# Optimization experiments

Measured on AMD Instinct MI355X. Metric: run time of the kernel, lower is better.

## Reference

```python
import jax, jax.numpy as jnp
import numpy as np

B, T, P, H, D = 2, 2048, 1024, 16, 128
C = H * D  # 2048
ROPE_THETA = 10000.0


def setup_inputs() -> dict:
    key = jax.random.key(0)
    ks = jax.random.split(key, 5)
    x = jax.random.normal(ks[0], (B, T, C), jnp.float32)
    w_qkv = jax.random.normal(ks[1], (C, 3 * C), jnp.float32) * 0.02  # Linear(dim, 3*dim), applied as x @ w
    w_out = jax.random.normal(ks[2], (C, C), jnp.float32) * 0.02
    past_k = jax.random.normal(ks[3], (B, H, P, D), jnp.float32)
    past_v = jax.random.normal(ks[4], (B, H, P, D), jnp.float32)
    return {"x": x, "w_qkv": w_qkv, "w_out": w_out, "past_k": past_k, "past_v": past_v}


def _rope(q, k, offset):
    # rotate-half RoPE (GPT-NeoX style), positions offset..offset+T-1
    d = q.shape[-1]
    inv_freq = 1.0 / (ROPE_THETA ** (jnp.arange(0, d, 2, dtype=jnp.float32) / d))  # [d/2]
    pos = offset + jnp.arange(q.shape[2], dtype=jnp.float32)                        # [T]
    ang = pos[:, None] * inv_freq[None, :]                                          # [T, d/2]
    cos = jnp.concatenate([jnp.cos(ang), jnp.cos(ang)], -1)[None, None]             # [1,1,T,d]
    sin = jnp.concatenate([jnp.sin(ang), jnp.sin(ang)], -1)[None, None]

    def rot_half(t):
        t1, t2 = jnp.split(t, 2, axis=-1)
        return jnp.concatenate([-t2, t1], -1)

    return q * cos + rot_half(q) * sin, k * cos + rot_half(k) * sin


def reference(x, w_qkv, w_out, past_k, past_v):
    Bv, Tv, Cv = x.shape
    Hn = past_k.shape[1]
    Dd = Cv // Hn
    # fused QKV projection
    qkv = x @ w_qkv                       # [B,T,3C]
    q, k, v = jnp.split(qkv, 3, axis=-1)  # each [B,T,C]

    def split_heads(t):
        return t.reshape(Bv, Tv, Hn, Dd).transpose(0, 2, 1, 3)  # [B,H,T,D]

    q, k, v = split_heads(q), split_heads(k), split_heads(v)
    # RoPE with offset = past length
    q, k = _rope(q, k, past_k.shape[2])
    # KV-cache concat along time axis
    k = jnp.concatenate([past_k, k], axis=2)  # [B,H,P+T,D]
    v = jnp.concatenate([past_v, v], axis=2)
    # SDPA: past_kv present -> is_causal=False, no mask (full attention)
    scale = 1.0 / jnp.sqrt(jnp.float32(Dd))
    scores = jnp.einsum('bhqd,bhkd->bhqk', q, k) * scale
    attn = jax.nn.softmax(scores, axis=-1)
    out = jnp.einsum('bhqk,bhkd->bhqd', attn, v)
    out = out.transpose(0, 2, 1, 3).reshape(Bv, Tv, Cv)
    return out @ w_out
```

## Files before the change

kernel.cpp:

```cpp
#include <hip/hip_runtime.h>
#include <stdint.h>

#define B_ 2
#define T_ 2048
#define P_ 1024
#define H_ 16
#define D_ 128
#define C_ 2048
#define S_ 3072
#define M_ 4096
#define N3_ 6144

typedef unsigned short u16;
typedef unsigned int uint32;
typedef __attribute__((ext_vector_type(8))) short short8;
typedef __attribute__((ext_vector_type(8))) __bf16 bf16x8;
typedef __attribute__((ext_vector_type(4))) float f32x4;
typedef __attribute__((ext_vector_type(16))) float f32x16;
typedef __attribute__((ext_vector_type(4))) unsigned short u16x4;
typedef __attribute__((ext_vector_type(4))) unsigned int uint4v;

static __device__ __forceinline__ float bf2f(u16 h) {
    union { unsigned int u; float f; } x; x.u = ((unsigned int)h) << 16; return x.f;
}
static __device__ __forceinline__ u16 f2bf(float f) {
    return __builtin_bit_cast(u16, (__bf16)f);
}
static __device__ __forceinline__ uint32 pkbf(float x, float y) {
    return (uint32)f2bf(x) | ((uint32)f2bf(y) << 16);
}

static __device__ __forceinline__ f32x4 mfma_bf16(short8 a, short8 b, f32x4 c) {
    return __builtin_amdgcn_mfma_f32_16x16x32_bf16(
        __builtin_bit_cast(bf16x8, a), __builtin_bit_cast(bf16x8, b), c, 0, 0, 0);
}
static __device__ __forceinline__ f32x16 mfma32(short8 a, short8 b, f32x16 c) {
    return __builtin_amdgcn_mfma_f32_32x32x16_bf16(
        __builtin_bit_cast(bf16x8, a), __builtin_bit_cast(bf16x8, b), c, 0, 0, 0);
}

typedef __attribute__((address_space(3))) unsigned int lds_u32;
typedef const __attribute__((address_space(1))) unsigned int glb_u32;
static __device__ __forceinline__ void gload_lds16(const void* g, void* l) {
    __builtin_amdgcn_global_load_lds((glb_u32*)g, (lds_u32*)l, 16, 0, 0);
}

static __device__ __forceinline__ void storeC(float* p, float v) { *p = v; }
static __device__ __forceinline__ void storeC(u16* p, float v) { *p = f2bf(v); }


__global__ void castx_kernel(const float* __restrict__ x, u16* __restrict__ Xb) {
    int idx = blockIdx.x * 256 + threadIdx.x;
    const float4 v = ((const float4*)x)[idx];
    u16x4 o;
    o.x = f2bf(v.x); o.y = f2bf(v.y); o.z = f2bf(v.z); o.w = f2bf(v.w);
    ((u16x4*)Xb)[idx] = o;
}

__global__ void wT_kernel(const float* __restrict__ W, u16* __restrict__ Wt,
                          int Ndim, int Kdim) {
    __shared__ float tile[64][65];
    const int n0 = blockIdx.x * 64, k0 = blockIdx.y * 64;
    const int tid = threadIdx.x;
#pragma unroll
    for (int i = 0; i < 16; i++) {
        int idx = tid + i * 256;
        int r = idx >> 6, c = idx & 63;
        tile[r][c] = W[(size_t)(k0 + r) * Ndim + n0 + c];
    }
    __syncthreads();
#pragma unroll
    for (int i = 0; i < 16; i++) {
        int idx = tid + i * 256;
        int r = idx >> 6, c = idx & 63;
        Wt[(size_t)(n0 + r) * Kdim + k0 + c] = f2bf(tile[c][r]);
    }
}

__global__ void rope_table_kernel(float* __restrict__ cosT, float* __restrict__ sinT) {
    int idx = blockIdx.x * 256 + threadIdx.x;
    int t = idx >> 6, d = idx & 63;
    float inv = powf(10000.0f, -(float)d * (1.0f / 64.0f));
    float ang = (float)(P_ + t) * inv;
    cosT[idx] = cosf(ang);
    sinT[idx] = sinf(ang);
}

__global__ void rope_qk_kernel(u16* __restrict__ QKVb, u16* __restrict__ Kc,
                               const float* __restrict__ cosT,
                               const float* __restrict__ sinT) {
    int idx = blockIdx.x * 256 + threadIdx.x;
    int d = idx & 63;
    int h = (idx >> 6) & 15;
    int t = (idx >> 10) & 2047;
    int b = idx >> 21;
    size_t rowoff = (size_t)(b * T_ + t) * N3_;
    float c = cosT[(t << 6) + d], s = sinT[(t << 6) + d];
    {
        u16* p1 = QKVb + rowoff + h * 128 + d;
        float x1 = bf2f(p1[0]), x2 = bf2f(p1[64]);
        p1[0]  = f2bf(x1 * c - x2 * s);
        p1[64] = f2bf(x2 * c + x1 * s);
    }
    {
        const u16* p1 = QKVb + rowoff + C_ + h * 128 + d;
        float x1 = bf2f(p1[0]), x2 = bf2f(p1[64]);
        u16* o = Kc + ((size_t)(b * H_ + h) * S_ + P_ + t) * 128 + d;
        o[0]  = f2bf(x1 * c - x2 * s);
        o[64] = f2bf(x2 * c + x1 * s);
    }
}

__global__ void pastk_kernel(const float* __restrict__ past_k, u16* __restrict__ Kc) {
    int idx = blockIdx.x * 256 + threadIdx.x;
    int d = idx & 127;
    int p = (idx >> 7) & 1023;
    int bh = idx >> 17;
    Kc[((size_t)bh * S_ + p) * 128 + d] = f2bf(past_k[idx]);
}

__global__ void vnewT_kernel(const u16* __restrict__ QKVb, u16* __restrict__ Vt) {
    __shared__ u16 tile[64][65];
    const int t0 = blockIdx.x * 64, d0 = blockIdx.y * 64, bh = blockIdx.z;
    const int b = bh >> 4, h = bh & 15;
    const int tid = threadIdx.x;
#pragma unroll
    for (int i = 0; i < 16; i++) {
        int idx = tid + i * 256;
        int r = idx >> 6, c = idx & 63;
        tile[r][c] = QKVb[(size_t)(b * T_ + t0 + r) * N3_ + 2 * C_ + h * 128 + d0 + c];
    }
    __syncthreads();
#pragma unroll
    for (int i = 0; i < 16; i++) {
        int idx = tid + i * 256;
        int r = idx >> 6, c = idx & 63;
        Vt[((size_t)bh * 128 + d0 + r) * S_ + P_ + t0 + c] = tile[c][r];
    }
}

__global__ void vpastT_kernel(const float* __restrict__ past_v, u16* __restrict__ Vt) {
    __shared__ float tile[64][65];
    const int p0 = blockIdx.x * 64, d0 = blockIdx.y * 64, bh = blockIdx.z;
    const int tid = threadIdx.x;
#pragma unroll
    for (int i = 0; i < 16; i++) {
        int idx = tid + i * 256;
        int r = idx >> 6, c = idx & 63;
        tile[r][c] = past_v[((size_t)bh * P_ + p0 + r) * 128 + d0 + c];
    }
    __syncthreads();
#pragma unroll
    for (int i = 0; i < 16; i++) {
        int idx = tid + i * 256;
        int r = idx >> 6, c = idx & 63;
        Vt[((size_t)bh * 128 + d0 + r) * S_ + p0 + c] = f2bf(tile[c][r]);
    }
}

template <typename OutT>
__global__ void __launch_bounds__(512, 1)
gemm3(const u16* __restrict__ A, const u16* __restrict__ Bt,
      OutT* __restrict__ Co, int Mdim, int Ndim, int Kdim) {
    __shared__ u16 lA[3 * 256 * 64];
    __shared__ u16 lB[3 * 128 * 64];
    const int nbx = Ndim >> 7;
    const int nwg = (Mdim >> 8) * nbx;
    int bid = blockIdx.x;
    int wg = (bid & 7) * (nwg >> 3) + (bid >> 3);
    const int bm = wg / nbx, bn = wg % nbx;
    const int m0 = bm << 8, n0 = bn << 7;
    const int tid = threadIdx.x;
    const int wave = tid >> 6, lane = tid & 63;
    const int mw = wave >> 1, nw = wave & 1;
    const int l15 = lane & 15, l4 = lane >> 4;

    f32x4 acc[4][4];
#pragma unroll
    for (int i = 0; i < 4; i++)
#pragma unroll
        for (int j = 0; j < 4; j++) acc[i][j] = (f32x4){0.f, 0.f, 0.f, 0.f};

    const u16* aSrc[4];
    const u16* bSrc[2];
#pragma unroll
    for (int i = 0; i < 4; i++) {
        int cid = i * 512 + tid;
        int r = cid >> 3, pc = cid & 7;
        aSrc[i] = A + (size_t)(m0 + r) * Kdim + ((pc ^ (r & 7)) << 3);
    }
#pragma unroll
    for (int i = 0; i < 2; i++) {
        int cid = i * 512 + tid;
        int r = cid >> 3, pc = cid & 7;
        bSrc[i] = Bt + (size_t)(n0 + r) * Kdim + ((pc ^ (r & 7)) << 3);
    }

#define STAGE3(bi, kt) do {                                                     \
    u16* _pa = lA + (bi) * 16384 + wave * 512;                                  \
    u16* _pb = lB + (bi) * 8192 + wave * 512;                                   \
    _Pragma("unroll")                                                           \
    for (int i = 0; i < 4; i++)                                                 \
        gload_lds16(aSrc[i] + (size_t)(kt) * 64, _pa + i * 4096);               \
    _Pragma("unroll")                                                           \
    for (int i = 0; i < 2; i++)                                                 \
        gload_lds16(bSrc[i] + (size_t)(kt) * 64, _pb + i * 4096);               \
} while (0)

    STAGE3(0, 0);
    STAGE3(1, 1);

    const int NT = Kdim >> 6;
    int bc = 0;
    for (int t = 0; t < NT; ++t) {
        if (t + 1 < NT) asm volatile("s_waitcnt vmcnt(6)" ::: "memory");
        else            asm volatile("s_waitcnt vmcnt(0)" ::: "memory");
        __builtin_amdgcn_s_barrier();
        asm volatile("" ::: "memory");
        if (t + 2 < NT) {
            int b2 = bc + 2; if (b2 >= 3) b2 -= 3;
            STAGE3(b2, t + 2);
        }
        const u16* la = lA + bc * 16384;
        const u16* lb = lB + bc * 8192;
        short8 af[4][2], bf[4][2];
#pragma unroll
        for (int i = 0; i < 4; i++)
#pragma unroll
            for (int kk = 0; kk < 2; kk++) {
                int r = mw * 64 + i * 16 + l15;
                int cb = (kk * 64 + l4 * 16) ^ ((r & 7) << 4);
                af[i][kk] = *(const short8*)&la[r * 64 + (cb >> 1)];
            }
#pragma unroll
        for (int j = 0; j < 4; j++)
#pragma unroll
            for (int kk = 0; kk < 2; kk++) {
                int r = nw * 64 + j * 16 + l15;
                int cb = (kk * 64 + l4 * 16) ^ ((r & 7) << 4);
                bf[j][kk] = *(const short8*)&lb[r * 64 + (cb >> 1)];
            }
        __builtin_amdgcn_s_setprio(1);
#pragma unroll
        for (int kk = 0; kk < 2; kk++)
#pragma unroll
            for (int i = 0; i < 4; i++)
#pragma unroll
                for (int j = 0; j < 4; j++)
                    acc[i][j] = mfma_bf16(af[i][kk], bf[j][kk], acc[i][j]);
        __builtin_amdgcn_s_setprio(0);
        __builtin_amdgcn_sched_barrier(0);
        bc = bc + 1; if (bc >= 3) bc = 0;
    }
#undef STAGE3

#pragma unroll
    for (int i = 0; i < 4; i++)
#pragma unroll
        for (int j = 0; j < 4; j++) {
            int row = m0 + mw * 64 + i * 16 + (l4 << 2);
            int col = n0 + nw * 64 + j * 16 + l15;
#pragma unroll
            for (int q = 0; q < 4; q++)
                storeC(&Co[(size_t)(row + q) * Ndim + col], acc[i][j][q]);
        }
}

__global__ void __launch_bounds__(256, 2)
attn_kernel(const u16* __restrict__ QKVb, const u16* __restrict__ Kc,
            const u16* __restrict__ Vt, u16* __restrict__ O) {
    __shared__ u16 ldsK[2][64 * 128];
    __shared__ u16 ldsV[2][128 * 64];

    int bid = blockIdx.x;
    int wg = (bid & 7) * 64 + (bid >> 3);
    const int qc = wg & 15;
    const int bh = wg >> 4;
    const int b = bh >> 4, h = bh & 15;
    const int tid = threadIdx.x, wave = tid >> 6, lane = tid & 63;
    const int l31 = lane & 31, hi = lane >> 5;

    const int krow = tid >> 4;
    const int kcol = (((tid & 15) << 4) ^ ((krow & 7) << 4)) >> 1;
    const int vrow = tid >> 3;
    const int vcol = (((tid & 7) << 4) ^ ((vrow & 7) << 4)) >> 1;

    const u16* Kbh = Kc + (size_t)bh * S_ * 128;
    const u16* Vbh = Vt + (size_t)bh * 128 * S_;

    const int tq = qc * 128 + wave * 32 + l31;
    short8 qf[8];
    {
        const u16* qp = QKVb + (size_t)(b * T_ + tq) * N3_ + h * 128 + hi * 8;
#pragma unroll
        for (int ks = 0; ks < 8; ks++) qf[ks] = *(const short8*)(qp + ks * 16);
    }

    f32x16 acco[4];
#pragma unroll
    for (int d = 0; d < 4; d++) acco[d] = (f32x16)(0.0f);
    float mrow = -1e30f, lrow = 0.f;
    const float sl2 = 0.08838834764831845f * 1.4426950408889634f;

#define STAGE(bufi, tt) do {                                                    \
    const int _s0 = (tt) * 64;                                                  \
    _Pragma("unroll")                                                           \
    for (int i = 0; i < 4; i++)                                                 \
        gload_lds16(Kbh + (size_t)(_s0 + krow + i * 16) * 128 + kcol,           \
                    (char*)&ldsK[bufi][0] + i * 4096 + wave * 1024);            \
    _Pragma("unroll")                                                           \
    for (int i = 0; i < 4; i++)                                                 \
        gload_lds16(Vbh + (size_t)(vrow + i * 32) * S_ + _s0 + vcol,            \
                    (char*)&ldsV[bufi][0] + i * 4096 + wave * 1024);            \
} while (0)

    STAGE(0, 0);
    __syncthreads();

    const int swz = (l31 & 7) << 4;

    for (int t = 0; t < S_ / 64; ++t) {
        const int cur = t & 1;
        if (t < S_ / 64 - 1) STAGE(cur ^ 1, t + 1);

        const u16* Kl = ldsK[cur];
        const u16* Vl = ldsV[cur];

        f32x16 p0 = (f32x16)(0.0f), p1 = (f32x16)(0.0f);
        __builtin_amdgcn_s_setprio(1);
#pragma unroll
        for (int ks = 0; ks < 8; ks++) {
            const int cidx = (((ks * 32 + hi * 16) ^ swz) >> 1);
            short8 k0 = *(const short8*)&Kl[(l31 << 7) + cidx];
            short8 k1 = *(const short8*)&Kl[((32 + l31) << 7) + cidx];
            p0 = mfma32(k0, qf[ks], p0);
            p1 = mfma32(k1, qf[ks], p1);
        }
        __builtin_amdgcn_s_setprio(0);

        float pm = fmaxf(p0[0], p0[1]);
#pragma unroll
        for (int r = 2; r < 16; r++) pm = fmaxf(pm, p0[r]);
#pragma unroll
        for (int r = 0; r < 16; r++) pm = fmaxf(pm, p1[r]);
        pm = fmaxf(pm, __shfl_xor(pm, 32));
        float pmS = pm * sl2;
        if (!__all(pmS <= mrow + 8.0f)) {
            float mn = fmaxf(mrow, pmS);
            float fac = exp2f(mrow - mn);
            mrow = mn;
            lrow *= fac;
#pragma unroll
            for (int d = 0; d < 4; d++)
#pragma unroll
                for (int r = 0; r < 16; r++) acco[d][r] *= fac;
        }
        float sum = 0.f;
#pragma unroll
        for (int r = 0; r < 16; r++) { p0[r] = exp2f(fmaf(p0[r], sl2, -mrow)); sum += p0[r]; }
#pragma unroll
        for (int r = 0; r < 16; r++) { p1[r] = exp2f(fmaf(p1[r], sl2, -mrow)); sum += p1[r]; }
        sum += __shfl_xor(sum, 32);
        lrow += sum;

        uint32 w[4][4];
#define PACK_HALF(pp, kh, ksout) do {                                           \
    uint32 A0 = pkbf(pp[(kh)*8 + 0], pp[(kh)*8 + 1]);                           \
    uint32 A1 = pkbf(pp[(kh)*8 + 2], pp[(kh)*8 + 3]);                           \
    uint32 B0 = pkbf(pp[(kh)*8 + 4], pp[(kh)*8 + 5]);                           \
    uint32 B1 = pkbf(pp[(kh)*8 + 6], pp[(kh)*8 + 7]);                           \
    uint32 sA0 = __shfl_xor(A0, 32), sA1 = __shfl_xor(A1, 32);                  \
    uint32 sB0 = __shfl_xor(B0, 32), sB1 = __shfl_xor(B1, 32);                  \
    w[ksout][0] = hi ? sB0 : A0;                                                \
    w[ksout][1] = hi ? sB1 : A1;                                                \
    w[ksout][2] = hi ? B0 : sA0;                                                \
    w[ksout][3] = hi ? B1 : sA1;                                                \
} while (0)
        PACK_HALF(p0, 0, 0);
        PACK_HALF(p0, 1, 1);
        PACK_HALF(p1, 0, 2);
        PACK_HALF(p1, 1, 3);
#undef PACK_HALF

        __builtin_amdgcn_s_setprio(1);
#pragma unroll
        for (int ks = 0; ks < 4; ks++) {
            uint4v pw = {w[ks][0], w[ks][1], w[ks][2], w[ks][3]};
            short8 pf = __builtin_bit_cast(short8, pw);
            const int cidx = (((ks * 32 + hi * 16) ^ swz) >> 1);
#pragma unroll
            for (int dblk = 0; dblk < 4; dblk++) {
                short8 vf = *(const short8*)&Vl[((dblk * 32 + l31) << 6) + cidx];
                acco[dblk] = mfma32(vf, pf, acco[dblk]);
            }
        }
        __builtin_amdgcn_s_setprio(0);

        __syncthreads();
    }
#undef STAGE

    float rl = 1.0f / lrow;
    u16* Op = O + (size_t)(b * T_ + tq) * C_ + h * 128;
#pragma unroll
    for (int dblk = 0; dblk < 4; dblk++)
#pragma unroll
        for (int j = 0; j < 4; j++) {
            u16x4 o;
            o.x = f2bf(acco[dblk][4 * j + 0] * rl);
            o.y = f2bf(acco[dblk][4 * j + 1] * rl);
            o.z = f2bf(acco[dblk][4 * j + 2] * rl);
            o.w = f2bf(acco[dblk][4 * j + 3] * rl);
            *(u16x4*)(Op + dblk * 32 + j * 8 + hi * 4) = o;
        }
}


extern "C" void kernel_launch(void* const* d_in, const int* in_sizes, int n_in,
                              void* d_out, int out_size, void* d_ws, size_t ws_size,
                              hipStream_t stream) {
    const float* x      = (const float*)d_in[0];
    const float* w_qkv  = (const float*)d_in[1];
    const float* w_out  = (const float*)d_in[2];
    const float* past_k = (const float*)d_in[3];
    const float* past_v = (const float*)d_in[4];
    float* out = (float*)d_out;

    char* ws = (char*)d_ws;
    u16* Xb    = (u16*)(ws);
    u16* Wqkvt = (u16*)(ws + 16777216);
    u16* Woutt = (u16*)(ws + 41943040);
    u16* QKVb  = (u16*)(ws + 50331648);
    u16* Kc    = (u16*)(ws + 100663296);
    u16* Vt    = (u16*)(ws + 125829120);
    u16* O     = (u16*)(ws + 150994944);
    float* cosT = (float*)(ws + 167772160);
    float* sinT = (float*)(ws + 168296448);

    castx_kernel<<<(M_ * C_ / 4) / 256, 256, 0, stream>>>(x, Xb);
    wT_kernel<<<dim3(N3_ / 64, C_ / 64), 256, 0, stream>>>(w_qkv, Wqkvt, N3_, C_);
    wT_kernel<<<dim3(C_ / 64, C_ / 64), 256, 0, stream>>>(w_out, Woutt, C_, C_);
    rope_table_kernel<<<(T_ * 64) / 256, 256, 0, stream>>>(cosT, sinT);

    gemm3<u16><<<(M_ / 256) * (N3_ / 128), 512, 0, stream>>>(Xb, Wqkvt, QKVb, M_, N3_, C_);

    rope_qk_kernel<<<(B_ * T_ * H_ * 64) / 256, 256, 0, stream>>>(QKVb, Kc, cosT, sinT);
    pastk_kernel<<<(B_ * H_ * P_ * D_) / 256, 256, 0, stream>>>(past_k, Kc);
    vnewT_kernel<<<dim3(T_ / 64, 2, B_ * H_), 256, 0, stream>>>(QKVb, Vt);
    vpastT_kernel<<<dim3(P_ / 64, 2, B_ * H_), 256, 0, stream>>>(past_v, Vt);

    attn_kernel<<<512, 256, 0, stream>>>(QKVb, Kc, Vt, O);

    gemm3<float><<<(M_ / 256) * (C_ / 128), 512, 0, stream>>>(O, Woutt, out, M_, C_, C_);
}
```

Measured before the change: 394.0 us.

## Use 32x32 MFMA in GEMM and tighten attention softmax instruction sequences

```diff
diff --git a/kernel.cpp b/kernel.cpp
--- a/kernel.cpp
+++ b/kernel.cpp
@@ -26,14 +26,13 @@
 static __device__ __forceinline__ u16 f2bf(float f) {
     return __builtin_bit_cast(u16, (__bf16)f);
 }
-static __device__ __forceinline__ uint32 pkbf(float x, float y) {
-    return (uint32)f2bf(x) | ((uint32)f2bf(y) << 16);
-}
-
-static __device__ __forceinline__ f32x4 mfma_bf16(short8 a, short8 b, f32x4 c) {
-    return __builtin_amdgcn_mfma_f32_16x16x32_bf16(
-        __builtin_bit_cast(bf16x8, a), __builtin_bit_cast(bf16x8, b), c, 0, 0, 0);
-}
+static __device__ __forceinline__ uint32 cvtpk(float lo, float hi) {
+    uint32 r;
+    asm("v_cvt_pk_bf16_f32 %0, %1, %2" : "=v"(r) : "v"(lo), "v"(hi));
+    return r;
+}
+#define MAX3(a, b, c) fmaxf(fmaxf((a), (b)), (c))
+
 static __device__ __forceinline__ f32x16 mfma32(short8 a, short8 b, f32x16 c) {
     return __builtin_amdgcn_mfma_f32_32x32x16_bf16(
         __builtin_bit_cast(bf16x8, a), __builtin_bit_cast(bf16x8, b), c, 0, 0, 0);
@@ -173,13 +172,13 @@
     const int tid = threadIdx.x;
     const int wave = tid >> 6, lane = tid & 63;
     const int mw = wave >> 1, nw = wave & 1;
-    const int l15 = lane & 15, l4 = lane >> 4;
-
-    f32x4 acc[4][4];
-#pragma unroll
-    for (int i = 0; i < 4; i++)
-#pragma unroll
-        for (int j = 0; j < 4; j++) acc[i][j] = (f32x4){0.f, 0.f, 0.f, 0.f};
+    const int l31 = lane & 31, hi = lane >> 5;
+
+    f32x16 acc[2][2];
+#pragma unroll
+    for (int i = 0; i < 2; i++)
+#pragma unroll
+        for (int j = 0; j < 2; j++) acc[i][j] = (f32x16)(0.0f);
 
     const u16* aSrc[4];
     const u16* bSrc[2];
@@ -223,31 +222,31 @@
         }
         const u16* la = lA + bc * 16384;
         const u16* lb = lB + bc * 8192;
-        short8 af[4][2], bf[4][2];
-#pragma unroll
-        for (int i = 0; i < 4; i++)
-#pragma unroll
-            for (int kk = 0; kk < 2; kk++) {
-                int r = mw * 64 + i * 16 + l15;
-                int cb = (kk * 64 + l4 * 16) ^ ((r & 7) << 4);
-                af[i][kk] = *(const short8*)&la[r * 64 + (cb >> 1)];
+        short8 af[2][4], bf[2][4];
+#pragma unroll
+        for (int mi = 0; mi < 2; mi++)
+#pragma unroll
+            for (int ks = 0; ks < 4; ks++) {
+                int r = mw * 64 + mi * 32 + l31;
+                int cb = ((ks << 5) + (hi << 4)) ^ ((r & 7) << 4);
+                af[mi][ks] = *(const short8*)&la[r * 64 + (cb >> 1)];
             }
 #pragma unroll
-        for (int j = 0; j < 4; j++)
-#pragma unroll
-            for (int kk = 0; kk < 2; kk++) {
-                int r = nw * 64 + j * 16 + l15;
-                int cb = (kk * 64 + l4 * 16) ^ ((r & 7) << 4);
-                bf[j][kk] = *(const short8*)&lb[r * 64 + (cb >> 1)];
+        for (int nj = 0; nj < 2; nj++)
+#pragma unroll
+            for (int ks = 0; ks < 4; ks++) {
+                int r = nw * 64 + nj * 32 + l31;
+                int cb = ((ks << 5) + (hi << 4)) ^ ((r & 7) << 4);
+                bf[nj][ks] = *(const short8*)&lb[r * 64 + (cb >> 1)];
             }
         __builtin_amdgcn_s_setprio(1);
 #pragma unroll
-        for (int kk = 0; kk < 2; kk++)
-#pragma unroll
-            for (int i = 0; i < 4; i++)
-#pragma unroll
-                for (int j = 0; j < 4; j++)
-                    acc[i][j] = mfma_bf16(af[i][kk], bf[j][kk], acc[i][j]);
+        for (int ks = 0; ks < 4; ks++)
+#pragma unroll
+            for (int mi = 0; mi < 2; mi++)
+#pragma unroll
+                for (int nj = 0; nj < 2; nj++)
+                    acc[mi][nj] = mfma32(af[mi][ks], bf[nj][ks], acc[mi][nj]);
         __builtin_amdgcn_s_setprio(0);
         __builtin_amdgcn_sched_barrier(0);
         bc = bc + 1; if (bc >= 3) bc = 0;
@@ -255,14 +254,18 @@
 #undef STAGE3
 
 #pragma unroll
-    for (int i = 0; i < 4; i++)
-#pragma unroll
-        for (int j = 0; j < 4; j++) {
-            int row = m0 + mw * 64 + i * 16 + (l4 << 2);
-            int col = n0 + nw * 64 + j * 16 + l15;
-#pragma unroll
-            for (int q = 0; q < 4; q++)
-                storeC(&Co[(size_t)(row + q) * Ndim + col], acc[i][j][q]);
+    for (int mi = 0; mi < 2; mi++)
+#pragma unroll
+        for (int nj = 0; nj < 2; nj++) {
+            int col = n0 + nw * 64 + nj * 32 + l31;
+#pragma unroll
+            for (int g = 0; g < 4; g++) {
+                int row = m0 + mw * 64 + mi * 32 + g * 8 + hi * 4;
+#pragma unroll
+                for (int q = 0; q < 4; q++)
+                    storeC(&Co[(size_t)(row + q) * Ndim + col],
+                           acc[mi][nj][g * 4 + q]);
+            }
         }
 }
 
@@ -338,11 +341,21 @@
         }
         __builtin_amdgcn_s_setprio(0);
 
-        float pm = fmaxf(p0[0], p0[1]);
-#pragma unroll
-        for (int r = 2; r < 16; r++) pm = fmaxf(pm, p0[r]);
-#pragma unroll
-        for (int r = 0; r < 16; r++) pm = fmaxf(pm, p1[r]);
+        float t0 = MAX3(p0[0], p0[1], p0[2]);
+        float t1 = MAX3(p0[3], p0[4], p0[5]);
+        float t2 = MAX3(p0[6], p0[7], p0[8]);
+        float t3 = MAX3(p0[9], p0[10], p0[11]);
+        float t4 = MAX3(p0[12], p0[13], p0[14]);
+        float t5 = MAX3(p0[15], p1[0], p1[1]);
+        float t6 = MAX3(p1[2], p1[3], p1[4]);
+        float t7 = MAX3(p1[5], p1[6], p1[7]);
+        float t8 = MAX3(p1[8], p1[9], p1[10]);
+        float t9 = MAX3(p1[11], p1[12], p1[13]);
+        float u0 = MAX3(t0, t1, t2);
+        float u1 = MAX3(t3, t4, t5);
+        float u2 = MAX3(t6, t7, t8);
+        float u3 = MAX3(t9, p1[14], p1[15]);
+        float pm = fmaxf(MAX3(u0, u1, u2), u3);
         pm = fmaxf(pm, __shfl_xor(pm, 32));
         float pmS = pm * sl2;
         if (!__all(pmS <= mrow + 8.0f)) {
@@ -355,20 +368,31 @@
 #pragma unroll
                 for (int r = 0; r < 16; r++) acco[d][r] *= fac;
         }
-        float sum = 0.f;
-#pragma unroll
-        for (int r = 0; r < 16; r++) { p0[r] = exp2f(fmaf(p0[r], sl2, -mrow)); sum += p0[r]; }
-#pragma unroll
-        for (int r = 0; r < 16; r++) { p1[r] = exp2f(fmaf(p1[r], sl2, -mrow)); sum += p1[r]; }
+        float s0 = 0.f, s1 = 0.f, s2 = 0.f, s3 = 0.f;
+#pragma unroll
+        for (int r = 0; r < 16; r += 4) {
+            p0[r + 0] = exp2f(fmaf(p0[r + 0], sl2, -mrow)); s0 += p0[r + 0];
+            p0[r + 1] = exp2f(fmaf(p0[r + 1], sl2, -mrow)); s1 += p0[r + 1];
+            p0[r + 2] = exp2f(fmaf(p0[r + 2], sl2, -mrow)); s2 += p0[r + 2];
+            p0[r + 3] = exp2f(fmaf(p0[r + 3], sl2, -mrow)); s3 += p0[r + 3];
+        }
+#pragma unroll
+        for (int r = 0; r < 16; r += 4) {
+            p1[r + 0] = exp2f(fmaf(p1[r + 0], sl2, -mrow)); s0 += p1[r + 0];
+            p1[r + 1] = exp2f(fmaf(p1[r + 1], sl2, -mrow)); s1 += p1[r + 1];
+            p1[r + 2] = exp2f(fmaf(p1[r + 2], sl2, -mrow)); s2 += p1[r + 2];
+            p1[r + 3] = exp2f(fmaf(p1[r + 3], sl2, -mrow)); s3 += p1[r + 3];
+        }
+        float sum = (s0 + s1) + (s2 + s3);
         sum += __shfl_xor(sum, 32);
         lrow += sum;
 
         uint32 w[4][4];
 #define PACK_HALF(pp, kh, ksout) do {                                           \
-    uint32 A0 = pkbf(pp[(kh)*8 + 0], pp[(kh)*8 + 1]);                           \
-    uint32 A1 = pkbf(pp[(kh)*8 + 2], pp[(kh)*8 + 3]);                           \
-    uint32 B0 = pkbf(pp[(kh)*8 + 4], pp[(kh)*8 + 5]);                           \
-    uint32 B1 = pkbf(pp[(kh)*8 + 6], pp[(kh)*8 + 7]);                           \
+    uint32 A0 = cvtpk(pp[(kh)*8 + 0], pp[(kh)*8 + 1]);                          \
+    uint32 A1 = cvtpk(pp[(kh)*8 + 2], pp[(kh)*8 + 3]);                          \
+    uint32 B0 = cvtpk(pp[(kh)*8 + 4], pp[(kh)*8 + 5]);                          \
+    uint32 B1 = cvtpk(pp[(kh)*8 + 6], pp[(kh)*8 + 7]);                          \
     uint32 sA0 = __shfl_xor(A0, 32), sA1 = __shfl_xor(A1, 32);                  \
     uint32 sB0 = __shfl_xor(B0, 32), sB1 = __shfl_xor(B1, 32);                  \
     w[ksout][0] = hi ? sB0 : A0;                                                \
```

Result: no change. 395.1 us (median of 2 runs) (+0.3%).
